# Kernel optimization log

Hardware: AMD Instinct MI355X
Metric: run time of the kernel (lower is better)

The kernel has to match this reference:

```python
import jax, jax.numpy as jnp
import numpy as np
import math

B, S, D, H = 4, 1024, 1024, 16
DH = D // H  # 64


def setup_inputs() -> dict:
    key = jax.random.key(0)
    ks = jax.random.split(key, 12)
    s = 0.02
    return {
        "hidden_states": jax.random.normal(ks[0], (B, S, D), jnp.float32),
        "attention_mask": jnp.zeros((B, 1, 1, S), jnp.float32),
        "context_embedded": jax.random.normal(ks[1], (B, S, D), jnp.float32),
        "Wq": s * jax.random.normal(ks[2], (D, D), jnp.float32),
        "bq": jnp.zeros((D,), jnp.float32),
        "Wk": s * jax.random.normal(ks[3], (D, D), jnp.float32),
        "bk": jnp.zeros((D,), jnp.float32),
        "Wv": s * jax.random.normal(ks[4], (D, D), jnp.float32),
        "bv": jnp.zeros((D,), jnp.float32),
        "Wcq": s * jax.random.normal(ks[5], (D, DH), jnp.float32),
        "bcq": jnp.zeros((DH,), jnp.float32),
        "Wck": s * jax.random.normal(ks[6], (D, DH), jnp.float32),
        "bck": jnp.zeros((DH,), jnp.float32),
        "w_lqc": s * jax.random.normal(ks[7], (DH,), jnp.float32),
        "w_lqq": s * jax.random.normal(ks[8], (DH,), jnp.float32),
        "w_lkc": s * jax.random.normal(ks[9], (DH,), jnp.float32),
        "w_lkk": s * jax.random.normal(ks[10], (DH,), jnp.float32),
    }


def _split_heads(x):
    b, s, _ = x.shape
    return x.reshape(b, s, H, DH).transpose(0, 2, 1, 3)  # [B,H,S,DH]


def reference(hidden_states, attention_mask, context_embedded,
              Wq, bq, Wk, bk, Wv, bv, Wcq, bcq, Wck, bck,
              w_lqc, w_lqq, w_lkc, w_lkk):
    scale = 1.0 / math.sqrt(DH)
    q = _split_heads(hidden_states @ Wq + bq)   # [B,H,S,DH]
    k = _split_heads(hidden_states @ Wk + bk)
    v = _split_heads(hidden_states @ Wv + bv)

    # standard attention
    scores = jnp.einsum('bhqd,bhkd->bhqk', q, k) * scale + attention_mask
    attention_probs = jax.nn.softmax(scores, axis=-1)  # [B,H,S,S]

    # context-derived quasi attention (head-invariant context projections)
    cq = context_embedded @ Wcq + bcq  # [B,S,DH]
    ck = context_embedded @ Wck + bck  # [B,S,DH]
    quasi_scores = jnp.einsum('bqd,bkd->bqk', cq, ck)[:, None] * scale  # [B,1,S,S]
    quasi_scores = jax.nn.sigmoid(quasi_scores + attention_mask)        # [B,H or 1,S,S]

    # sigmoid lambda gates
    lambda_q = jax.nn.sigmoid((cq @ w_lqc)[:, None, :, None] + jnp.einsum('bhsd,d->bhs', q, w_lqq)[..., None])  # [B,H,S,1]
    lambda_k = jax.nn.sigmoid((ck @ w_lkc)[:, None, :, None] + jnp.einsum('bhsd,d->bhs', k, w_lkk)[..., None])  # [B,H,S,1]
    lambda_context = 1.0 - (lambda_q + lambda_k)  # [B,H,S,1]

    quasi_attention_prob = lambda_context * quasi_scores          # [B,H,S,S]
    new_attention_probs = attention_probs + quasi_attention_prob  # [B,H,S,S]

    ctx = jnp.einsum('bhqk,bhkd->bhqd', new_attention_probs, v)   # [B,H,S,DH]
    ctx = ctx.transpose(0, 2, 1, 3).reshape(B, S, D)
    return (ctx, new_attention_probs, attention_probs, quasi_attention_prob)
```

## Files before the change

kernel.cpp:

```cpp
#include <hip/hip_runtime.h>
#include <hip/hip_bf16.h>

static constexpr int B_ = 4;
static constexpr int S_ = 1024;
static constexpr int D_ = 1024;
static constexpr int H_ = 16;
static constexpr int DH_ = 64;
static constexpr float SCALE = 0.125f;

__device__ __forceinline__ float sigm(float x) { return 1.0f / (1.0f + __expf(-x)); }

__global__ __launch_bounds__(256) void gemm_qkv(
    const float* __restrict__ A,
    const float* __restrict__ Wq, const float* __restrict__ bq,
    const float* __restrict__ Wk, const float* __restrict__ bk,
    const float* __restrict__ Wv, const float* __restrict__ bv,
    float* __restrict__ qo, float* __restrict__ ko, float* __restrict__ vo)
{
    __shared__ float At[32][64];
    __shared__ float Bs[32][64];
    const int t  = threadIdx.x;
    const int bx = blockIdx.x;
    const int by = blockIdx.y;
    const int mat   = bx >> 4;
    const int ncol0 = (bx & 15) * 64;
    const float* W   = (mat == 0) ? Wq : (mat == 1) ? Wk : Wv;
    const float* bi  = (mat == 0) ? bq : (mat == 1) ? bk : bv;
    float*       out = (mat == 0) ? qo : (mat == 1) ? ko : vo;

    const int tx = t & 15, ty = t >> 4;
    const int ar = t >> 3, ac = (t & 7) << 2;
    const int br = t >> 4, bc = (t & 15) << 2;

    float acc[4][4] = {};
    for (int k0 = 0; k0 < D_; k0 += 32) {
        float4 a0 = *(const float4*)(A + (size_t)(by * 64 + ar) * D_ + k0 + ac);
        float4 a1 = *(const float4*)(A + (size_t)(by * 64 + ar + 32) * D_ + k0 + ac);
        float4 b0 = *(const float4*)(W + (size_t)(k0 + br) * D_ + ncol0 + bc);
        float4 b1 = *(const float4*)(W + (size_t)(k0 + br + 16) * D_ + ncol0 + bc);
        At[ac + 0][ar] = a0.x; At[ac + 1][ar] = a0.y;
        At[ac + 2][ar] = a0.z; At[ac + 3][ar] = a0.w;
        At[ac + 0][ar + 32] = a1.x; At[ac + 1][ar + 32] = a1.y;
        At[ac + 2][ar + 32] = a1.z; At[ac + 3][ar + 32] = a1.w;
        *(float4*)(&Bs[br][bc])      = b0;
        *(float4*)(&Bs[br + 16][bc]) = b1;
        __syncthreads();
        #pragma unroll
        for (int kk = 0; kk < 32; ++kk) {
            float4 avv = *(const float4*)(&At[kk][ty * 4]);
            float4 bvv = *(const float4*)(&Bs[kk][tx * 4]);
            const float* av = reinterpret_cast<const float*>(&avv);
            const float* bv = reinterpret_cast<const float*>(&bvv);
            #pragma unroll
            for (int i = 0; i < 4; ++i)
                #pragma unroll
                for (int j = 0; j < 4; ++j)
                    acc[i][j] = fmaf(av[i], bv[j], acc[i][j]);
        }
        __syncthreads();
    }
    const int hh = ncol0 >> 6;
    #pragma unroll
    for (int i = 0; i < 4; ++i) {
        int m  = by * 64 + ty * 4 + i;
        int bb = m >> 10, ss = m & (S_ - 1);
        float* dst = out + ((size_t)(bb * H_ + hh) * S_ + ss) * DH_ + tx * 4;
        float4 ov;
        ((float*)&ov)[0] = acc[i][0] + bi[ncol0 + tx * 4 + 0];
        ((float*)&ov)[1] = acc[i][1] + bi[ncol0 + tx * 4 + 1];
        ((float*)&ov)[2] = acc[i][2] + bi[ncol0 + tx * 4 + 2];
        ((float*)&ov)[3] = acc[i][3] + bi[ncol0 + tx * 4 + 3];
        *(float4*)dst = ov;
    }
}

__global__ __launch_bounds__(256) void gemm_cqck(
    const float* __restrict__ A,
    const float* __restrict__ Wcq, const float* __restrict__ bcq,
    const float* __restrict__ Wck, const float* __restrict__ bck,
    float* __restrict__ cqo, float* __restrict__ cko)
{
    __shared__ float At[32][64];
    __shared__ float Bs[32][64];
    const int t  = threadIdx.x;
    const int bx = blockIdx.x;
    const int by = blockIdx.y;
    const float* W   = bx ? Wck : Wcq;
    const float* bi  = bx ? bck : bcq;
    float*       out = bx ? cko : cqo;

    const int tx = t & 15, ty = t >> 4;
    const int ar = t >> 3, ac = (t & 7) << 2;
    const int br = t >> 4, bc = (t & 15) << 2;

    float acc[4][4] = {};
    for (int k0 = 0; k0 < D_; k0 += 32) {
        float4 a0 = *(const float4*)(A + (size_t)(by * 64 + ar) * D_ + k0 + ac);
        float4 a1 = *(const float4*)(A + (size_t)(by * 64 + ar + 32) * D_ + k0 + ac);
        float4 b0 = *(const float4*)(W + (size_t)(k0 + br) * DH_ + bc);
        float4 b1 = *(const float4*)(W + (size_t)(k0 + br + 16) * DH_ + bc);
        At[ac + 0][ar] = a0.x; At[ac + 1][ar] = a0.y;
        At[ac + 2][ar] = a0.z; At[ac + 3][ar] = a0.w;
        At[ac + 0][ar + 32] = a1.x; At[ac + 1][ar + 32] = a1.y;
        At[ac + 2][ar + 32] = a1.z; At[ac + 3][ar + 32] = a1.w;
        *(float4*)(&Bs[br][bc])      = b0;
        *(float4*)(&Bs[br + 16][bc]) = b1;
        __syncthreads();
        #pragma unroll
        for (int kk = 0; kk < 32; ++kk) {
            float4 avv = *(const float4*)(&At[kk][ty * 4]);
            float4 bvv = *(const float4*)(&Bs[kk][tx * 4]);
            const float* av = reinterpret_cast<const float*>(&avv);
            const float* bv = reinterpret_cast<const float*>(&bvv);
            #pragma unroll
            for (int i = 0; i < 4; ++i)
                #pragma unroll
                for (int j = 0; j < 4; ++j)
                    acc[i][j] = fmaf(av[i], bv[j], acc[i][j]);
        }
        __syncthreads();
    }
    #pragma unroll
    for (int i = 0; i < 4; ++i) {
        int m = by * 64 + ty * 4 + i;
        float4 ov;
        ((float*)&ov)[0] = acc[i][0] + bi[tx * 4 + 0];
        ((float*)&ov)[1] = acc[i][1] + bi[tx * 4 + 1];
        ((float*)&ov)[2] = acc[i][2] + bi[tx * 4 + 2];
        ((float*)&ov)[3] = acc[i][3] + bi[tx * 4 + 3];
        *(float4*)(out + (size_t)m * DH_ + tx * 4) = ov;
    }
}

__global__ __launch_bounds__(256) void lambda_kernel(
    const float* __restrict__ q, const float* __restrict__ k,
    const float* __restrict__ cq, const float* __restrict__ ck,
    const float* __restrict__ wlqc, const float* __restrict__ wlqq,
    const float* __restrict__ wlkc, const float* __restrict__ wlkk,
    float* __restrict__ lam)
{
    __shared__ float w[4][64];
    const int t = threadIdx.x;
    if (t < 64) { w[0][t] = wlqc[t]; w[1][t] = wlqq[t]; w[2][t] = wlkc[t]; w[3][t] = wlkk[t]; }
    __syncthreads();
    const int idx = blockIdx.x * 256 + t;
    const int ssi = idx & (S_ - 1);
    const int bh  = idx >> 10;
    const int b   = bh >> 4;
    const float* qrow  = q  + (size_t)idx * DH_;
    const float* krow  = k  + (size_t)idx * DH_;
    const float* cqrow = cq + ((size_t)b * S_ + ssi) * DH_;
    const float* ckrow = ck + ((size_t)b * S_ + ssi) * DH_;
    float s1 = 0.f, s2 = 0.f, s3 = 0.f, s4 = 0.f;
    #pragma unroll 8
    for (int d = 0; d < DH_; ++d) {
        s1 = fmaf(cqrow[d], w[0][d], s1);
        s2 = fmaf(qrow[d],  w[1][d], s2);
        s3 = fmaf(ckrow[d], w[2][d], s3);
        s4 = fmaf(krow[d],  w[3][d], s4);
    }
    lam[idx] = 1.0f - sigm(s1 + s2) - sigm(s3 + s4);
}

__global__ __launch_bounds__(256) void score64(
    const float* __restrict__ Abase, const float* __restrict__ Bbase,
    float* __restrict__ Obase, const float* __restrict__ mask,
    int bshift, int do_sig)
{
    __shared__ float At[64][64];
    __shared__ float Bt[64][64];
    const int z  = blockIdx.z;
    const int jt = blockIdx.x, it = blockIdx.y;
    const float* Am = Abase + (size_t)z * S_ * DH_;
    const float* Bm = Bbase + (size_t)z * S_ * DH_;
    float*       Om = Obase + (size_t)z * S_ * S_;
    const int b = z >> bshift;
    const int t = threadIdx.x;
    const int r = t >> 2, c0 = (t & 3) << 4;
    #pragma unroll
    for (int u = 0; u < 4; ++u) {
        float4 av = *(const float4*)(Am + (size_t)(it * 64 + r) * DH_ + c0 + u * 4);
        float4 bv = *(const float4*)(Bm + (size_t)(jt * 64 + r) * DH_ + c0 + u * 4);
        At[c0 + u * 4 + 0][r] = av.x; At[c0 + u * 4 + 1][r] = av.y;
        At[c0 + u * 4 + 2][r] = av.z; At[c0 + u * 4 + 3][r] = av.w;
        Bt[c0 + u * 4 + 0][r] = bv.x; Bt[c0 + u * 4 + 1][r] = bv.y;
        Bt[c0 + u * 4 + 2][r] = bv.z; Bt[c0 + u * 4 + 3][r] = bv.w;
    }
    __syncthreads();
    const int tx = t & 15, ty = t >> 4;
    float acc[4][4] = {};
    #pragma unroll 8
    for (int d = 0; d < 64; ++d) {
        float4 avv = *(const float4*)(&At[d][ty * 4]);
        float4 bvv = *(const float4*)(&Bt[d][tx * 4]);
        const float* av = reinterpret_cast<const float*>(&avv);
        const float* bv = reinterpret_cast<const float*>(&bvv);
        #pragma unroll
        for (int i = 0; i < 4; ++i)
            #pragma unroll
            for (int j = 0; j < 4; ++j)
                acc[i][j] = fmaf(av[i], bv[j], acc[i][j]);
    }
    #pragma unroll
    for (int i = 0; i < 4; ++i) {
        const int ig = it * 64 + ty * 4 + i;
        float4 ov;
        #pragma unroll
        for (int j = 0; j < 4; ++j) {
            const int jg = jt * 64 + tx * 4 + j;
            float val = acc[i][j] * SCALE + mask[b * S_ + jg];
            if (do_sig) val = sigm(val);
            ((float*)&ov)[j] = val;
        }
        *(float4*)(&Om[(size_t)ig * S_ + jt * 64 + tx * 4]) = ov;
    }
}

__global__ __launch_bounds__(256) void softmax_merge(
    float* __restrict__ attn, float* __restrict__ newp, float* __restrict__ quasi,
    const float* __restrict__ qs, const float* __restrict__ lam)
{
    __shared__ float red[256];
    const int row = blockIdx.x;
    const int t   = threadIdx.x;
    const int i   = row & (S_ - 1);
    const int bh  = row >> 10;
    const int b   = bh >> 4;
    float* arow = attn + (size_t)row * S_;
    float4 x = *(const float4*)(arow + t * 4);
    float m = fmaxf(fmaxf(x.x, x.y), fmaxf(x.z, x.w));
    red[t] = m; __syncthreads();
    for (int s = 128; s > 0; s >>= 1) {
        if (t < s) red[t] = fmaxf(red[t], red[t + s]);
        __syncthreads();
    }
    m = red[0]; __syncthreads();
    float4 e;
    e.x = __expf(x.x - m); e.y = __expf(x.y - m);
    e.z = __expf(x.z - m); e.w = __expf(x.w - m);
    red[t] = e.x + e.y + e.z + e.w; __syncthreads();
    for (int s = 128; s > 0; s >>= 1) {
        if (t < s) red[t] += red[t + s];
        __syncthreads();
    }
    const float inv = 1.0f / red[0];
    float4 p; p.x = e.x * inv; p.y = e.y * inv; p.z = e.z * inv; p.w = e.w * inv;
    *(float4*)(arow + t * 4) = p;

    const float l = lam[row];
    float4 qv = *(const float4*)(qs + ((size_t)b * S_ + i) * S_ + t * 4);
    float4 qp; qp.x = l * qv.x; qp.y = l * qv.y; qp.z = l * qv.z; qp.w = l * qv.w;
    float4 nv; nv.x = p.x + qp.x; nv.y = p.y + qp.y; nv.z = p.z + qp.z; nv.w = p.w + qp.w;
    *(float4*)(quasi + (size_t)row * S_ + t * 4) = qp;
    *(float4*)(newp  + (size_t)row * S_ + t * 4) = nv;
}

__global__ __launch_bounds__(256) void gemm_ctx(
    const float* __restrict__ P, const float* __restrict__ Vm, float* __restrict__ ctx)
{
    __shared__ float At[32][64];
    __shared__ float Bs[32][64];
    const int by = blockIdx.x;
    const int bh = blockIdx.y;
    const float* Ap = P  + (size_t)bh * S_ * S_;
    const float* Bp = Vm + (size_t)bh * S_ * DH_;
    const int t = threadIdx.x;
    const int tx = t & 15, ty = t >> 4;
    const int ar = t >> 3, ac = (t & 7) << 2;
    const int br = t >> 4, bc = (t & 15) << 2;

    float acc[4][4] = {};
    for (int k0 = 0; k0 < S_; k0 += 32) {
        float4 a0 = *(const float4*)(Ap + (size_t)(by * 64 + ar) * S_ + k0 + ac);
        float4 a1 = *(const float4*)(Ap + (size_t)(by * 64 + ar + 32) * S_ + k0 + ac);
        float4 b0 = *(const float4*)(Bp + (size_t)(k0 + br) * DH_ + bc);
        float4 b1 = *(const float4*)(Bp + (size_t)(k0 + br + 16) * DH_ + bc);
        At[ac + 0][ar] = a0.x; At[ac + 1][ar] = a0.y;
        At[ac + 2][ar] = a0.z; At[ac + 3][ar] = a0.w;
        At[ac + 0][ar + 32] = a1.x; At[ac + 1][ar + 32] = a1.y;
        At[ac + 2][ar + 32] = a1.z; At[ac + 3][ar + 32] = a1.w;
        *(float4*)(&Bs[br][bc])      = b0;
        *(float4*)(&Bs[br + 16][bc]) = b1;
        __syncthreads();
        #pragma unroll
        for (int kk = 0; kk < 32; ++kk) {
            float4 avv = *(const float4*)(&At[kk][ty * 4]);
            float4 bvv = *(const float4*)(&Bs[kk][tx * 4]);
            const float* av = reinterpret_cast<const float*>(&avv);
            const float* bv = reinterpret_cast<const float*>(&bvv);
            #pragma unroll
            for (int i = 0; i < 4; ++i)
                #pragma unroll
                for (int j = 0; j < 4; ++j)
                    acc[i][j] = fmaf(av[i], bv[j], acc[i][j]);
        }
        __syncthreads();
    }
    const int b = bh >> 4, h = bh & 15;
    #pragma unroll
    for (int i = 0; i < 4; ++i) {
        const int srow = by * 64 + ty * 4 + i;
        float4 ov;
        ((float*)&ov)[0] = acc[i][0]; ((float*)&ov)[1] = acc[i][1];
        ((float*)&ov)[2] = acc[i][2]; ((float*)&ov)[3] = acc[i][3];
        *(float4*)(ctx + ((size_t)b * S_ + srow) * D_ + h * DH_ + tx * 4) = ov;
    }
}

extern "C" void kernel_launch(void* const* d_in, const int* in_sizes, int n_in,
                              void* d_out, int out_size, void* d_ws, size_t ws_size,
                              hipStream_t stream) {
    const float* hs   = (const float*)d_in[0];
    const float* mask = (const float*)d_in[1];
    const float* ce   = (const float*)d_in[2];
    const float* Wq   = (const float*)d_in[3];
    const float* bq   = (const float*)d_in[4];
    const float* Wk   = (const float*)d_in[5];
    const float* bk   = (const float*)d_in[6];
    const float* Wv   = (const float*)d_in[7];
    const float* bv   = (const float*)d_in[8];
    const float* Wcq  = (const float*)d_in[9];
    const float* bcq  = (const float*)d_in[10];
    const float* Wck  = (const float*)d_in[11];
    const float* bck  = (const float*)d_in[12];
    const float* wlqc = (const float*)d_in[13];
    const float* wlqq = (const float*)d_in[14];
    const float* wlkc = (const float*)d_in[15];
    const float* wlkk = (const float*)d_in[16];

    float* out   = (float*)d_out;
    float* ctx   = out;
    float* newp  = ctx  + (size_t)B_ * S_ * D_;
    float* attn  = newp + (size_t)B_ * H_ * S_ * S_;
    float* quasi = attn + (size_t)B_ * H_ * S_ * S_;

    float* ws = (float*)d_ws;
    float* q  = ws;
    float* k  = q  + (size_t)B_ * H_ * S_ * DH_;
    float* v  = k  + (size_t)B_ * H_ * S_ * DH_;
    float* cq = v  + (size_t)B_ * H_ * S_ * DH_;
    float* ck = cq + (size_t)B_ * S_ * DH_;
    float* lam = ck + (size_t)B_ * S_ * DH_;
    float* qs  = lam + (size_t)B_ * H_ * S_;

    gemm_qkv<<<dim3(48, 64), 256, 0, stream>>>(hs, Wq, bq, Wk, bk, Wv, bv, q, k, v);
    gemm_cqck<<<dim3(2, 64), 256, 0, stream>>>(ce, Wcq, bcq, Wck, bck, cq, ck);
    lambda_kernel<<<256, 256, 0, stream>>>(q, k, cq, ck, wlqc, wlqq, wlkc, wlkk, lam);
    score64<<<dim3(16, 16, 4), 256, 0, stream>>>(cq, ck, qs, mask, 0, 1);
    score64<<<dim3(16, 16, 64), 256, 0, stream>>>(q, k, attn, mask, 4, 0);
    softmax_merge<<<65536, 256, 0, stream>>>(attn, newp, quasi, qs, lam);
    gemm_ctx<<<dim3(16, 64), 256, 0, stream>>>(newp, v, ctx);
}
```

Before: 1.558 ms.

## Use bf16 MFMA for QKV projection and fuse attention scores, softmax, merge, and PV

Hidden states and weights are cast to bf16 (weights transposed), and the QKV projection now runs on 16x16x32 bf16 MFMA instructions with bf16 outputs. A new fused attention kernel computes QK^T with MFMA, does the softmax in registers, writes the three probability outputs, and multiplies the bf16 merged probabilities by a transposed V using MFMA. This removes the fp32 score write and re-read, the separate softmax pass, and the fp32 SIMT GEMMs. In exchange it lowers precision to bf16 for Q, K, V and the probabilities used in the PV product, and it adds extra cast and transpose kernels.

```diff
diff --git a/kernel.cpp b/kernel.cpp
--- a/kernel.cpp
+++ b/kernel.cpp
@@ -1,5 +1,8 @@
 #include <hip/hip_runtime.h>
-#include <hip/hip_bf16.h>
+
+typedef __attribute__((ext_vector_type(8))) short s16x8;
+typedef __attribute__((ext_vector_type(4))) short s16x4;
+typedef __attribute__((ext_vector_type(4))) float f32x4;
 
 static constexpr int B_ = 4;
 static constexpr int S_ = 1024;
@@ -10,23 +13,114 @@
 
 __device__ __forceinline__ float sigm(float x) { return 1.0f / (1.0f + __expf(-x)); }
 
-__global__ __launch_bounds__(256) void gemm_qkv(
+__device__ __forceinline__ unsigned short f2b(float f) {
+    unsigned int u = __float_as_uint(f);
+    return (unsigned short)((u + 0x7FFFu + ((u >> 16) & 1u)) >> 16);
+}
+__device__ __forceinline__ float b2f(unsigned short u) {
+    return __uint_as_float(((unsigned int)u) << 16);
+}
+
+__global__ __launch_bounds__(256) void cast_bf16(const float* __restrict__ in,
+                                                 short* __restrict__ out) {
+    const size_t idx = (size_t)blockIdx.x * 256 + threadIdx.x;
+    float4 x = *(const float4*)(in + idx * 4);
+    s16x4 o;
+    o[0] = (short)f2b(x.x); o[1] = (short)f2b(x.y);
+    o[2] = (short)f2b(x.z); o[3] = (short)f2b(x.w);
+    *(s16x4*)(out + idx * 4) = o;
+}
+
+__global__ __launch_bounds__(256) void transpose_cast_w(
+    const float* __restrict__ Wq, const float* __restrict__ Wk,
+    const float* __restrict__ Wv, short* __restrict__ Wt) {
+    __shared__ float tile[32][33];
+    const float* W = (blockIdx.z == 0) ? Wq : (blockIdx.z == 1) ? Wk : Wv;
+    short* dst = Wt + (size_t)blockIdx.z * 1024 * 1024;
+    const int t = threadIdx.x, tx = t & 31, ty = t >> 5;
+    const int n0 = blockIdx.x * 32, k0 = blockIdx.y * 32;
+    #pragma unroll
+    for (int r = 0; r < 4; ++r)
+        tile[ty + 8 * r][tx] = W[(size_t)(k0 + ty + 8 * r) * 1024 + n0 + tx];
+    __syncthreads();
+    #pragma unroll
+    for (int r = 0; r < 4; ++r)
+        dst[(size_t)(n0 + ty + 8 * r) * 1024 + k0 + tx] =
+            (short)f2b(tile[tx][ty + 8 * r]);
+}
+
+__global__ __launch_bounds__(256) void gemm_qkv_mfma(
+    const short* __restrict__ hsb, const short* __restrict__ Wt,
+    const float* __restrict__ bq, const float* __restrict__ bk,
+    const float* __restrict__ bv,
+    short* __restrict__ qb, short* __restrict__ kb, short* __restrict__ vb) {
+    const int t = threadIdx.x;
+    const int w = t >> 6, l = t & 63;
+    const int lg = l >> 4, ll = l & 15;
+    const int bx = blockIdx.x, by = blockIdx.y;
+    const int mat = bx >> 4;
+    const int ncol0 = (bx & 15) * 64;
+    const float* bias = (mat == 0) ? bq : (mat == 1) ? bk : bv;
+    short* dst = (mat == 0) ? qb : (mat == 1) ? kb : vb;
+    const short* Wm = Wt + (size_t)mat * 1024 * 1024;
+
+    const short* Aptr = hsb + (size_t)(by * 64 + w * 16 + ll) * 1024 + lg * 8;
+    const short* Bptr = Wm + (size_t)(ncol0 + ll) * 1024 + lg * 8;
+
+    f32x4 zero = {0.f, 0.f, 0.f, 0.f};
+    f32x4 acc[4] = {zero, zero, zero, zero};
+    for (int k0 = 0; k0 < 1024; k0 += 32) {
+        s16x8 a = *(const s16x8*)(Aptr + k0);
+        #pragma unroll
+        for (int jt = 0; jt < 4; ++jt) {
+            s16x8 b = *(const s16x8*)(Bptr + (size_t)jt * 16 * 1024 + k0);
+            acc[jt] = __builtin_amdgcn_mfma_f32_16x16x32_bf16(a, b, acc[jt], 0, 0, 0);
+        }
+    }
+    const int h = bx & 15;
+    #pragma unroll
+    for (int jt = 0; jt < 4; ++jt) {
+        const int d = jt * 16 + ll;
+        const float bsum = bias[ncol0 + d];
+        #pragma unroll
+        for (int r = 0; r < 4; ++r) {
+            const int m = by * 64 + w * 16 + lg * 4 + r;
+            const int bb = m >> 10, ss = m & (S_ - 1);
+            dst[(((size_t)(bb * H_ + h)) * S_ + ss) * DH_ + d] =
+                (short)f2b(acc[jt][r] + bsum);
+        }
+    }
+}
+
+__global__ __launch_bounds__(256) void transpose_v(const short* __restrict__ v,
+                                                   short* __restrict__ vt) {
+    __shared__ short tile[64][72];
+    const int bh = blockIdx.y, s0 = blockIdx.x * 64;
+    const int t = threadIdx.x, tx = t & 63, ty = t >> 6;
+    const short* src = v + (size_t)bh * S_ * DH_;
+    short* dst = vt + (size_t)bh * DH_ * S_;
+    #pragma unroll
+    for (int r = 0; r < 16; ++r)
+        tile[ty + 4 * r][tx] = src[(size_t)(s0 + ty + 4 * r) * DH_ + tx];
+    __syncthreads();
+    #pragma unroll
+    for (int r = 0; r < 16; ++r)
+        dst[(size_t)(ty + 4 * r) * S_ + s0 + tx] = tile[tx][ty + 4 * r];
+}
+
+__global__ __launch_bounds__(256) void gemm_cqck(
     const float* __restrict__ A,
-    const float* __restrict__ Wq, const float* __restrict__ bq,
-    const float* __restrict__ Wk, const float* __restrict__ bk,
-    const float* __restrict__ Wv, const float* __restrict__ bv,
-    float* __restrict__ qo, float* __restrict__ ko, float* __restrict__ vo)
-{
+    const float* __restrict__ Wcq, const float* __restrict__ bcq,
+    const float* __restrict__ Wck, const float* __restrict__ bck,
+    float* __restrict__ cqo, float* __restrict__ cko) {
     __shared__ float At[32][64];
     __shared__ float Bs[32][64];
-    const int t  = threadIdx.x;
+    const int t = threadIdx.x;
     const int bx = blockIdx.x;
     const int by = blockIdx.y;
-    const int mat   = bx >> 4;
-    const int ncol0 = (bx & 15) * 64;
-    const float* W   = (mat == 0) ? Wq : (mat == 1) ? Wk : Wv;
-    const float* bi  = (mat == 0) ? bq : (mat == 1) ? bk : bv;
-    float*       out = (mat == 0) ? qo : (mat == 1) ? ko : vo;
+    const float* W = bx ? Wck : Wcq;
+    const float* bi = bx ? bck : bcq;
+    float* out = bx ? cko : cqo;
 
     const int tx = t & 15, ty = t >> 4;
     const int ar = t >> 3, ac = (t & 7) << 2;
@@ -36,13 +130,13 @@
     for (int k0 = 0; k0 < D_; k0 += 32) {
         float4 a0 = *(const float4*)(A + (size_t)(by * 64 + ar) * D_ + k0 + ac);
         float4 a1 = *(const float4*)(A + (size_t)(by * 64 + ar + 32) * D_ + k0 + ac);
-        float4 b0 = *(const float4*)(W + (size_t)(k0 + br) * D_ + ncol0 + bc);
-        float4 b1 = *(const float4*)(W + (size_t)(k0 + br + 16) * D_ + ncol0 + bc);
+        float4 b0 = *(const float4*)(W + (size_t)(k0 + br) * DH_ + bc);
+        float4 b1 = *(const float4*)(W + (size_t)(k0 + br + 16) * DH_ + bc);
         At[ac + 0][ar] = a0.x; At[ac + 1][ar] = a0.y;
         At[ac + 2][ar] = a0.z; At[ac + 3][ar] = a0.w;
         At[ac + 0][ar + 32] = a1.x; At[ac + 1][ar + 32] = a1.y;
         At[ac + 2][ar + 32] = a1.z; At[ac + 3][ar + 32] = a1.w;
-        *(float4*)(&Bs[br][bc])      = b0;
+        *(float4*)(&Bs[br][bc]) = b0;
         *(float4*)(&Bs[br + 16][bc]) = b1;
         __syncthreads();
         #pragma unroll
@@ -59,67 +153,6 @@
         }
         __syncthreads();
     }
-    const int hh = ncol0 >> 6;
-    #pragma unroll
-    for (int i = 0; i < 4; ++i) {
-        int m  = by * 64 + ty * 4 + i;
-        int bb = m >> 10, ss = m & (S_ - 1);
-        float* dst = out + ((size_t)(bb * H_ + hh) * S_ + ss) * DH_ + tx * 4;
-        float4 ov;
-        ((float*)&ov)[0] = acc[i][0] + bi[ncol0 + tx * 4 + 0];
-        ((float*)&ov)[1] = acc[i][1] + bi[ncol0 + tx * 4 + 1];
-        ((float*)&ov)[2] = acc[i][2] + bi[ncol0 + tx * 4 + 2];
-        ((float*)&ov)[3] = acc[i][3] + bi[ncol0 + tx * 4 + 3];
-        *(float4*)dst = ov;
-    }
-}
-
-__global__ __launch_bounds__(256) void gemm_cqck(
-    const float* __restrict__ A,
-    const float* __restrict__ Wcq, const float* __restrict__ bcq,
-    const float* __restrict__ Wck, const float* __restrict__ bck,
-    float* __restrict__ cqo, float* __restrict__ cko)
-{
-    __shared__ float At[32][64];
-    __shared__ float Bs[32][64];
-    const int t  = threadIdx.x;
-    const int bx = blockIdx.x;
-    const int by = blockIdx.y;
-    const float* W   = bx ? Wck : Wcq;
-    const float* bi  = bx ? bck : bcq;
-    float*       out = bx ? cko : cqo;
-
-    const int tx = t & 15, ty = t >> 4;
-    const int ar = t >> 3, ac = (t & 7) << 2;
-    const int br = t >> 4, bc = (t & 15) << 2;
-
-    float acc[4][4] = {};
-    for (int k0 = 0; k0 < D_; k0 += 32) {
-        float4 a0 = *(const float4*)(A + (size_t)(by * 64 + ar) * D_ + k0 + ac);
-        float4 a1 = *(const float4*)(A + (size_t)(by * 64 + ar + 32) * D_ + k0 + ac);
-        float4 b0 = *(const float4*)(W + (size_t)(k0 + br) * DH_ + bc);
-        float4 b1 = *(const float4*)(W + (size_t)(k0 + br + 16) * DH_ + bc);
-        At[ac + 0][ar] = a0.x; At[ac + 1][ar] = a0.y;
-        At[ac + 2][ar] = a0.z; At[ac + 3][ar] = a0.w;
-        At[ac + 0][ar + 32] = a1.x; At[ac + 1][ar + 32] = a1.y;
-        At[ac + 2][ar + 32] = a1.z; At[ac + 3][ar + 32] = a1.w;
-        *(float4*)(&Bs[br][bc])      = b0;
-        *(float4*)(&Bs[br + 16][bc]) = b1;
-        __syncthreads();
-        #pragma unroll
-        for (int kk = 0; kk < 32; ++kk) {
-            float4 avv = *(const float4*)(&At[kk][ty * 4]);
-            float4 bvv = *(const float4*)(&Bs[kk][tx * 4]);
-            const float* av = reinterpret_cast<const float*>(&avv);
-            const float* bv = reinterpret_cast<const float*>(&bvv);
-            #pragma unroll
-            for (int i = 0; i < 4; ++i)
-                #pragma unroll
-                for (int j = 0; j < 4; ++j)
-                    acc[i][j] = fmaf(av[i], bv[j], acc[i][j]);
-        }
-        __syncthreads();
-    }
     #pragma unroll
     for (int i = 0; i < 4; ++i) {
         int m = by * 64 + ty * 4 + i;
@@ -133,31 +166,34 @@
 }
 
 __global__ __launch_bounds__(256) void lambda_kernel(
-    const float* __restrict__ q, const float* __restrict__ k,
+    const short* __restrict__ q, const short* __restrict__ k,
     const float* __restrict__ cq, const float* __restrict__ ck,
     const float* __restrict__ wlqc, const float* __restrict__ wlqq,
     const float* __restrict__ wlkc, const float* __restrict__ wlkk,
-    float* __restrict__ lam)
-{
+    float* __restrict__ lam) {
     __shared__ float w[4][64];
     const int t = threadIdx.x;
     if (t < 64) { w[0][t] = wlqc[t]; w[1][t] = wlqq[t]; w[2][t] = wlkc[t]; w[3][t] = wlkk[t]; }
     __syncthreads();
     const int idx = blockIdx.x * 256 + t;
     const int ssi = idx & (S_ - 1);
-    const int bh  = idx >> 10;
-    const int b   = bh >> 4;
-    const float* qrow  = q  + (size_t)idx * DH_;
-    const float* krow  = k  + (size_t)idx * DH_;
+    const int b = idx >> 14;
+    const short* qrow = q + (size_t)idx * DH_;
+    const short* krow = k + (size_t)idx * DH_;
     const float* cqrow = cq + ((size_t)b * S_ + ssi) * DH_;
     const float* ckrow = ck + ((size_t)b * S_ + ssi) * DH_;
     float s1 = 0.f, s2 = 0.f, s3 = 0.f, s4 = 0.f;
-    #pragma unroll 8
-    for (int d = 0; d < DH_; ++d) {
-        s1 = fmaf(cqrow[d], w[0][d], s1);
-        s2 = fmaf(qrow[d],  w[1][d], s2);
-        s3 = fmaf(ckrow[d], w[2][d], s3);
-        s4 = fmaf(krow[d],  w[3][d], s4);
+    #pragma unroll
+    for (int d0 = 0; d0 < DH_; d0 += 8) {
+        s16x8 qa = *(const s16x8*)(qrow + d0);
+        s16x8 ka = *(const s16x8*)(krow + d0);
+        #pragma unroll
+        for (int e = 0; e < 8; ++e) {
+            s1 = fmaf(cqrow[d0 + e], w[0][d0 + e], s1);
+            s2 = fmaf(b2f((unsigned short)qa[e]), w[1][d0 + e], s2);
+            s3 = fmaf(ckrow[d0 + e], w[2][d0 + e], s3);
+            s4 = fmaf(b2f((unsigned short)ka[e]), w[3][d0 + e], s4);
+        }
     }
     lam[idx] = 1.0f - sigm(s1 + s2) - sigm(s3 + s4);
 }
@@ -165,15 +201,14 @@
 __global__ __launch_bounds__(256) void score64(
     const float* __restrict__ Abase, const float* __restrict__ Bbase,
     float* __restrict__ Obase, const float* __restrict__ mask,
-    int bshift, int do_sig)
-{
+    int bshift, int do_sig) {
     __shared__ float At[64][64];
     __shared__ float Bt[64][64];
-    const int z  = blockIdx.z;
+    const int z = blockIdx.z;
     const int jt = blockIdx.x, it = blockIdx.y;
     const float* Am = Abase + (size_t)z * S_ * DH_;
     const float* Bm = Bbase + (size_t)z * S_ * DH_;
-    float*       Om = Obase + (size_t)z * S_ * S_;
+    float* Om = Obase + (size_t)z * S_ * S_;
     const int b = z >> bshift;
     const int t = threadIdx.x;
     const int r = t >> 2, c0 = (t & 3) << 4;
@@ -216,94 +251,149 @@
     }
 }
 
-__global__ __launch_bounds__(256) void softmax_merge(
-    float* __restrict__ attn, float* __restrict__ newp, float* __restrict__ quasi,
-    const float* __restrict__ qs, const float* __restrict__ lam)
-{
-    __shared__ float red[256];
-    const int row = blockIdx.x;
-    const int t   = threadIdx.x;
-    const int i   = row & (S_ - 1);
-    const int bh  = row >> 10;
-    const int b   = bh >> 4;
-    float* arow = attn + (size_t)row * S_;
-    float4 x = *(const float4*)(arow + t * 4);
-    float m = fmaxf(fmaxf(x.x, x.y), fmaxf(x.z, x.w));
-    red[t] = m; __syncthreads();
-    for (int s = 128; s > 0; s >>= 1) {
-        if (t < s) red[t] = fmaxf(red[t], red[t + s]);
-        __syncthreads();
-    }
-    m = red[0]; __syncthreads();
-    float4 e;
-    e.x = __expf(x.x - m); e.y = __expf(x.y - m);
-    e.z = __expf(x.z - m); e.w = __expf(x.w - m);
-    red[t] = e.x + e.y + e.z + e.w; __syncthreads();
-    for (int s = 128; s > 0; s >>= 1) {
-        if (t < s) red[t] += red[t + s];
-        __syncthreads();
-    }
-    const float inv = 1.0f / red[0];
-    float4 p; p.x = e.x * inv; p.y = e.y * inv; p.z = e.z * inv; p.w = e.w * inv;
-    *(float4*)(arow + t * 4) = p;
-
-    const float l = lam[row];
-    float4 qv = *(const float4*)(qs + ((size_t)b * S_ + i) * S_ + t * 4);
-    float4 qp; qp.x = l * qv.x; qp.y = l * qv.y; qp.z = l * qv.z; qp.w = l * qv.w;
-    float4 nv; nv.x = p.x + qp.x; nv.y = p.y + qp.y; nv.z = p.z + qp.z; nv.w = p.w + qp.w;
-    *(float4*)(quasi + (size_t)row * S_ + t * 4) = qp;
-    *(float4*)(newp  + (size_t)row * S_ + t * 4) = nv;
-}
-
-__global__ __launch_bounds__(256) void gemm_ctx(
-    const float* __restrict__ P, const float* __restrict__ Vm, float* __restrict__ ctx)
-{
-    __shared__ float At[32][64];
-    __shared__ float Bs[32][64];
-    const int by = blockIdx.x;
+__global__ __launch_bounds__(256) void attn_fused(
+    const short* __restrict__ qb, const short* __restrict__ kb,
+    const short* __restrict__ vt, const float* __restrict__ qs,
+    const float* __restrict__ lam, const float* __restrict__ mask,
+    float* __restrict__ attn, float* __restrict__ quasi,
+    float* __restrict__ newp, float* __restrict__ ctx) {
+    __shared__ short Plds[16][1032];
+    __shared__ float ctxred[4][16][64];
+    __shared__ float redm[4][16];
+    __shared__ float reds[4][16];
+
+    const int t = threadIdx.x;
+    const int w = t >> 6, l = t & 63;
+    const int lg = l >> 4, ll = l & 15;
+    const int i0 = blockIdx.x * 16;
     const int bh = blockIdx.y;
-    const float* Ap = P  + (size_t)bh * S_ * S_;
-    const float* Bp = Vm + (size_t)bh * S_ * DH_;
-    const int t = threadIdx.x;
-    const int tx = t & 15, ty = t >> 4;
-    const int ar = t >> 3, ac = (t & 7) << 2;
-    const int br = t >> 4, bc = (t & 15) << 2;
-
-    float acc[4][4] = {};
-    for (int k0 = 0; k0 < S_; k0 += 32) {
-        float4 a0 = *(const float4*)(Ap + (size_t)(by * 64 + ar) * S_ + k0 + ac);
-        float4 a1 = *(const float4*)(Ap + (size_t)(by * 64 + ar + 32) * S_ + k0 + ac);
-        float4 b0 = *(const float4*)(Bp + (size_t)(k0 + br) * DH_ + bc);
-        float4 b1 = *(const float4*)(Bp + (size_t)(k0 + br + 16) * DH_ + bc);
-        At[ac + 0][ar] = a0.x; At[ac + 1][ar] = a0.y;
-        At[ac + 2][ar] = a0.z; At[ac + 3][ar] = a0.w;
-        At[ac + 0][ar + 32] = a1.x; At[ac + 1][ar + 32] = a1.y;
-        At[ac + 2][ar + 32] = a1.z; At[ac + 3][ar + 32] = a1.w;
-        *(float4*)(&Bs[br][bc])      = b0;
-        *(float4*)(&Bs[br + 16][bc]) = b1;
-        __syncthreads();
-        #pragma unroll
-        for (int kk = 0; kk < 32; ++kk) {
-            float4 avv = *(const float4*)(&At[kk][ty * 4]);
-            float4 bvv = *(const float4*)(&Bs[kk][tx * 4]);
-            const float* av = reinterpret_cast<const float*>(&avv);
-            const float* bv = reinterpret_cast<const float*>(&bvv);
-            #pragma unroll
-            for (int i = 0; i < 4; ++i)
-                #pragma unroll
-                for (int j = 0; j < 4; ++j)
-                    acc[i][j] = fmaf(av[i], bv[j], acc[i][j]);
-        }
-        __syncthreads();
-    }
     const int b = bh >> 4, h = bh & 15;
-    #pragma unroll
-    for (int i = 0; i < 4; ++i) {
-        const int srow = by * 64 + ty * 4 + i;
-        float4 ov;
-        ((float*)&ov)[0] = acc[i][0]; ((float*)&ov)[1] = acc[i][1];
-        ((float*)&ov)[2] = acc[i][2]; ((float*)&ov)[3] = acc[i][3];
-        *(float4*)(ctx + ((size_t)b * S_ + srow) * D_ + h * DH_ + tx * 4) = ov;
+
+    const short* qp = qb + (((size_t)bh * S_) + i0 + ll) * DH_ + lg * 8;
+    s16x8 aq0 = *(const s16x8*)(qp);
+    s16x8 aq1 = *(const s16x8*)(qp + 32);
+
+    f32x4 acc[16];
+    const short* kp0 = kb + (((size_t)bh * S_) + w * 256 + ll) * DH_ + lg * 8;
+    #pragma unroll
+    for (int jt = 0; jt < 16; ++jt) {
+        const short* kp = kp0 + (size_t)jt * 16 * DH_;
+        s16x8 b0 = *(const s16x8*)(kp);
+        s16x8 b1 = *(const s16x8*)(kp + 32);
+        f32x4 c = {0.f, 0.f, 0.f, 0.f};
+        c = __builtin_amdgcn_mfma_f32_16x16x32_bf16(aq0, b0, c, 0, 0, 0);
+        c = __builtin_amdgcn_mfma_f32_16x16x32_bf16(aq1, b1, c, 0, 0, 0);
+        acc[jt] = c;
+    }
+
+    float rmax[4] = {-3.0e38f, -3.0e38f, -3.0e38f, -3.0e38f};
+    #pragma unroll
+    for (int jt = 0; jt < 16; ++jt) {
+        float mk = mask[b * S_ + w * 256 + jt * 16 + ll];
+        #pragma unroll
+        for (int r = 0; r < 4; ++r) {
+            float sv = acc[jt][r] * SCALE + mk;
+            acc[jt][r] = sv;
+            rmax[r] = fmaxf(rmax[r], sv);
+        }
+    }
+    #pragma unroll
+    for (int off = 1; off < 16; off <<= 1)
+        #pragma unroll
+        for (int r = 0; r < 4; ++r)
+            rmax[r] = fmaxf(rmax[r], __shfl_xor(rmax[r], off));
+    if (ll == 0) {
+        #pragma unroll
+        for (int r = 0; r < 4; ++r) redm[w][lg * 4 + r] = rmax[r];
+    }
+    __syncthreads();
+    #pragma unroll
+    for (int r = 0; r < 4; ++r) {
+        const int row = lg * 4 + r;
+        rmax[r] = fmaxf(fmaxf(redm[0][row], redm[1][row]),
+                        fmaxf(redm[2][row], redm[3][row]));
+    }
+
+    float rsum[4] = {0.f, 0.f, 0.f, 0.f};
+    #pragma unroll
+    for (int jt = 0; jt < 16; ++jt)
+        #pragma unroll
+        for (int r = 0; r < 4; ++r) {
+            float e = __expf(acc[jt][r] - rmax[r]);
+            acc[jt][r] = e;
+            rsum[r] += e;
+        }
+    #pragma unroll
+    for (int off = 1; off < 16; off <<= 1)
+        #pragma unroll
+        for (int r = 0; r < 4; ++r)
+            rsum[r] += __shfl_xor(rsum[r], off);
+    if (ll == 0) {
+        #pragma unroll
+        for (int r = 0; r < 4; ++r) reds[w][lg * 4 + r] = rsum[r];
+    }
+    __syncthreads();
+
+    float inv[4], lamr[4];
+    size_t obase[4], qsbase[4];
+    #pragma unroll
+    for (int r = 0; r < 4; ++r) {
+        const int row = lg * 4 + r;
+        inv[r] = 1.0f / (reds[0][row] + reds[1][row] + reds[2][row] + reds[3][row]);
+        const int rg = i0 + row;
+        lamr[r] = lam[(size_t)bh * S_ + rg];
+        obase[r] = ((size_t)bh * S_ + rg) * S_;
+        qsbase[r] = ((size_t)b * S_ + rg) * S_;
+    }
+
+    #pragma unroll
+    for (int jt = 0; jt < 16; ++jt) {
+        const int col = w * 256 + jt * 16 + ll;
+        #pragma unroll
+        for (int r = 0; r < 4; ++r) {
+            float p = acc[jt][r] * inv[r];
+            float qv = qs[qsbase[r] + col];
+            float qp_ = lamr[r] * qv;
+            float np = p + qp_;
+            attn[obase[r] + col] = p;
+            quasi[obase[r] + col] = qp_;
+            newp[obase[r] + col] = np;
+            Plds[lg * 4 + r][col] = (short)f2b(np);
+        }
+    }
+    __syncthreads();
+
+    f32x4 zero = {0.f, 0.f, 0.f, 0.f};
+    f32x4 cacc[4] = {zero, zero, zero, zero};
+    const short* vp0 = vt + ((size_t)bh * DH_ + ll) * S_ + w * 256 + lg * 8;
+    #pragma unroll
+    for (int ks = 0; ks < 8; ++ks) {
+        s16x8 a = *(const s16x8*)(&Plds[ll][w * 256 + ks * 32 + lg * 8]);
+        #pragma unroll
+        for (int jd = 0; jd < 4; ++jd) {
+            s16x8 bv = *(const s16x8*)(vp0 + (size_t)jd * 16 * S_ + ks * 32);
+            cacc[jd] = __builtin_amdgcn_mfma_f32_16x16x32_bf16(a, bv, cacc[jd], 0, 0, 0);
+        }
+    }
+    #pragma unroll
+    for (int jd = 0; jd < 4; ++jd)
+        #pragma unroll
+        for (int r = 0; r < 4; ++r)
+            ctxred[w][lg * 4 + r][jd * 16 + ll] = cacc[jd][r];
+    __syncthreads();
+
+    {
+        const int r = t >> 4, c = (t & 15) * 4;
+        float4 s0 = *(const float4*)&ctxred[0][r][c];
+        float4 s1 = *(const float4*)&ctxred[1][r][c];
+        float4 s2 = *(const float4*)&ctxred[2][r][c];
+        float4 s3 = *(const float4*)&ctxred[3][r][c];
+        float4 o;
+        o.x = s0.x + s1.x + s2.x + s3.x;
+        o.y = s0.y + s1.y + s2.y + s3.y;
+        o.z = s0.z + s1.z + s2.z + s3.z;
+        o.w = s0.w + s1.w + s2.w + s3.w;
+        *(float4*)(ctx + ((size_t)b * S_ + i0 + r) * D_ + h * DH_ + c) = o;
     }
 }
 
@@ -334,20 +424,24 @@
     float* attn  = newp + (size_t)B_ * H_ * S_ * S_;
     float* quasi = attn + (size_t)B_ * H_ * S_ * S_;
 
-    float* ws = (float*)d_ws;
-    float* q  = ws;
-    float* k  = q  + (size_t)B_ * H_ * S_ * DH_;
-    float* v  = k  + (size_t)B_ * H_ * S_ * DH_;
-    float* cq = v  + (size_t)B_ * H_ * S_ * DH_;
-    float* ck = cq + (size_t)B_ * S_ * DH_;
-    float* lam = ck + (size_t)B_ * S_ * DH_;
-    float* qs  = lam + (size_t)B_ * H_ * S_;
-
-    gemm_qkv<<<dim3(48, 64), 256, 0, stream>>>(hs, Wq, bq, Wk, bk, Wv, bv, q, k, v);
+    short* hsb = (short*)d_ws;
+    short* Wt  = hsb + (size_t)4096 * 1024;
+    short* qb  = Wt  + (size_t)3 * 1024 * 1024;
+    short* kb  = qb  + (size_t)4096 * 1024;
+    short* vb  = kb  + (size_t)4096 * 1024;
+    short* vtb = vb  + (size_t)4096 * 1024;
+    float* cq  = (float*)(vtb + (size_t)4096 * 1024);
+    float* ck  = cq + (size_t)B_ * S_ * DH_;
+    float* lamp = ck + (size_t)B_ * S_ * DH_;
+    float* qsp  = lamp + (size_t)B_ * H_ * S_;
+
+    cast_bf16<<<dim3(4096), 256, 0, stream>>>(hs, hsb);
+    transpose_cast_w<<<dim3(32, 32, 3), 256, 0, stream>>>(Wq, Wk, Wv, Wt);
+    gemm_qkv_mfma<<<dim3(48, 64), 256, 0, stream>>>(hsb, Wt, bq, bk, bv, qb, kb, vb);
+    transpose_v<<<dim3(16, 64), 256, 0, stream>>>(vb, vtb);
     gemm_cqck<<<dim3(2, 64), 256, 0, stream>>>(ce, Wcq, bcq, Wck, bck, cq, ck);
-    lambda_kernel<<<256, 256, 0, stream>>>(q, k, cq, ck, wlqc, wlqq, wlkc, wlkk, lam);
-    score64<<<dim3(16, 16, 4), 256, 0, stream>>>(cq, ck, qs, mask, 0, 1);
-    score64<<<dim3(16, 16, 64), 256, 0, stream>>>(q, k, attn, mask, 4, 0);
-    softmax_merge<<<65536, 256, 0, stream>>>(attn, newp, quasi, qs, lam);
-    gemm_ctx<<<dim3(16, 64), 256, 0, stream>>>(newp, v, ctx);
-}
+    lambda_kernel<<<256, 256, 0, stream>>>(qb, kb, cq, ck, wlqc, wlqq, wlkc, wlkk, lamp);
+    score64<<<dim3(16, 16, 4), 256, 0, stream>>>(cq, ck, qsp, mask, 0, 1);
+    attn_fused<<<dim3(64, 64), 256, 0, stream>>>(qb, kb, vtb, qsp, lamp, mask,
+                                                 attn, quasi, newp, ctx);
+}
```

Result: faster. 1.330 ms (-14.7%).
